# Kernel optimization log

Hardware: AMD Instinct MI355X
Metric: run time of the kernel (lower is better)

Reference implementation:

```python
import jax, jax.numpy as jnp
import numpy as np

D_MODEL = 1024
H = 16
D_K = D_MODEL // H

def setup_inputs() -> dict:
    key = jax.random.key(0)
    ks = jax.random.split(key, 7)
    B, S = 4, 2048
    q = jax.random.normal(ks[0], (B, S, D_MODEL), dtype=jnp.float32)
    k = jax.random.normal(ks[1], (B, S, D_MODEL), dtype=jnp.float32)
    v = jax.random.normal(ks[2], (B, S, D_MODEL), dtype=jnp.float32)
    scale = 1.0 / np.sqrt(D_MODEL)
    w_q = jax.random.normal(ks[3], (D_MODEL, D_MODEL), dtype=jnp.float32) * scale
    w_k = jax.random.normal(ks[4], (D_MODEL, D_MODEL), dtype=jnp.float32) * scale
    w_v = jax.random.normal(ks[5], (D_MODEL, D_MODEL), dtype=jnp.float32) * scale
    w_o = jax.random.normal(ks[6], (D_MODEL, D_MODEL), dtype=jnp.float32) * scale
    return {"q": q, "k": k, "v": v, "w_q": w_q, "w_k": w_k, "w_v": w_v, "w_o": w_o}

def reference(q, k, v, w_q, w_k, w_v, w_o):
    B, S, _ = q.shape
    # Linear layers (no bias): x @ W^T, weights stored torch-style [out, in]
    def proj(x, w):
        y = jnp.einsum('bsd,ed->bse', x, w)
        return y.reshape(B, -1, H, D_K).transpose(0, 2, 1, 3)  # [B,H,S,d_k]
    query = proj(q, w_q)
    key_ = proj(k, w_k)
    value = proj(v, w_v)
    scores = jnp.einsum('bhqd,bhkd->bhqk', query, key_) / jnp.sqrt(jnp.float32(D_K))
    attn = jax.nn.softmax(scores, axis=-1)  # dropout p=0 -> identity
    x = jnp.einsum('bhqk,bhkd->bhqd', attn, value)
    x = x.transpose(0, 2, 1, 3).reshape(B, S, H * D_K)
    return jnp.einsum('bsd,ed->bse', x, w_o)
```

## Files before the change

kernel.cpp:

```cpp
#include <hip/hip_runtime.h>

typedef unsigned short ushort_t;
typedef __attribute__((ext_vector_type(8))) short bf16x8;
typedef __attribute__((ext_vector_type(4))) float f32x4;
typedef __attribute__((ext_vector_type(16))) float f32x16;
typedef __attribute__((ext_vector_type(4))) unsigned short ushort4v;
typedef __attribute__((ext_vector_type(4))) unsigned int uint4v;

__device__ __forceinline__ ushort_t f2bf(float f) {
  unsigned u = __float_as_uint(f);
  u += 0x7FFFu + ((u >> 16) & 1u);
  return (ushort_t)(u >> 16);
}

__device__ __forceinline__ unsigned cvt_pk(float lo, float hi) {
  unsigned r;
  asm("v_cvt_pk_bf16_f32 %0, %1, %2" : "=v"(r) : "v"(lo), "v"(hi));
  return r;
}

__device__ __forceinline__ float fast_exp2(float x) {
  float r;
  asm("v_exp_f32 %0, %1" : "=v"(r) : "v"(x));
  return r;
}

__device__ __forceinline__ void gload16(ushort_t* lds, const ushort_t* g) {
  __builtin_amdgcn_global_load_lds(
      (const __attribute__((address_space(1))) unsigned int*)g,
      (__attribute__((address_space(3))) unsigned int*)lds, 16, 0, 0);
}

__global__ void cast_w4(const float* __restrict__ s0, const float* __restrict__ s1,
                        const float* __restrict__ s2, const float* __restrict__ s3,
                        ushort_t* __restrict__ dst, int n4) {
  int i = blockIdx.x * blockDim.x + threadIdx.x;
  if (i >= n4) return;
  int z = blockIdx.y;
  const float* s = (z == 0) ? s0 : (z == 1) ? s1 : (z == 2) ? s2 : s3;
  float4 f = ((const float4*)s)[i];
  ushort4v o;
  o.x = f2bf(f.x); o.y = f2bf(f.y); o.z = f2bf(f.z); o.w = f2bf(f.w);
  ((ushort4v*)(dst + (size_t)z * n4 * 4))[i] = o;
}

__global__ __launch_bounds__(256, 2)
void qkv_gemm(const float* __restrict__ qa, const float* __restrict__ ka,
              const float* __restrict__ va, const ushort_t* __restrict__ Wb,
              ushort_t* __restrict__ QKp, ushort_t* __restrict__ Vt,
              float qscale) {
  const int M = 8192, N = 1024, K = 1024;
  __shared__ __align__(16) ushort_t As[2][128 * 64];
  __shared__ __align__(16) ushort_t Bs[2][128 * 64];
  const int tid = threadIdx.x;
  const int wave = tid >> 6, lane = tid & 63;
  const int wr = wave >> 1, wc = wave & 1;
  const int frow = lane & 15, g = lane >> 4;
  const int r8 = lane >> 3, c8 = lane & 7;
  const int m0 = blockIdx.x * 128, n0 = blockIdx.y * 128;
  const int z = blockIdx.z;

  const float* Asrc = (z == 0) ? qa : (z == 1) ? ka : va;
  const float scale = (z == 0) ? qscale : 1.0f;

  f32x4 acc[4][4] = {};

  const int sc = (c8 ^ r8) << 3;
  const ushort_t* Bb = Wb + (size_t)z * N * K + (size_t)(n0 + wave * 32 + r8) * K + sc;
  const float* Af = Asrc + (size_t)(m0 + wave * 32 + r8) * K + sc;

  float aF[32];
  auto loadA = [&](int t) {
#pragma unroll
    for (int j = 0; j < 4; ++j) {
      *(float4*)&aF[j * 8]     = *(const float4*)(Af + (size_t)j * 8 * K + t * 64);
      *(float4*)&aF[j * 8 + 4] = *(const float4*)(Af + (size_t)j * 8 * K + t * 64 + 4);
    }
  };
  auto writeA = [&](int sel) {
    ushort_t* AsW = &As[sel][(wave * 32) * 64];
#pragma unroll
    for (int j = 0; j < 4; ++j) {
      uint4v w;
      w[0] = cvt_pk(aF[j * 8 + 0], aF[j * 8 + 1]);
      w[1] = cvt_pk(aF[j * 8 + 2], aF[j * 8 + 3]);
      w[2] = cvt_pk(aF[j * 8 + 4], aF[j * 8 + 5]);
      w[3] = cvt_pk(aF[j * 8 + 6], aF[j * 8 + 7]);
      *(uint4v*)&AsW[j * 8 * 64 + lane * 8] = w;
    }
  };
  auto stageB = [&](int t, int sel) {
    ushort_t* BsW = &Bs[sel][(wave * 32) * 64];
#pragma unroll
    for (int j = 0; j < 4; ++j)
      gload16(BsW + j * 8 * 64, Bb + (size_t)j * 8 * K + t * 64);
  };

  loadA(0);
  writeA(0);
  stageB(0, 0);
  loadA(1);
  __syncthreads();

  const int NT = K / 64;
  for (int t = 0; t < NT; ++t) {
    const int cur = t & 1, nxt = cur ^ 1;
    if (t < NT - 1) {
      writeA(nxt);
      stageB(t + 1, nxt);
      if (t < NT - 2) loadA(t + 2);
    }

    bf16x8 af[4][2], bfr[4][2];
#pragma unroll
    for (int mi = 0; mi < 4; ++mi) {
      int row = wr * 64 + mi * 16 + frow;
#pragma unroll
      for (int ki = 0; ki < 2; ++ki)
        af[mi][ki] = *(const bf16x8*)&As[cur][row * 64 + (((ki * 4 + g) ^ (row & 7)) << 3)];
    }
#pragma unroll
    for (int nf = 0; nf < 4; ++nf) {
      int row = wc * 64 + nf * 16 + frow;
#pragma unroll
      for (int ki = 0; ki < 2; ++ki)
        bfr[nf][ki] = *(const bf16x8*)&Bs[cur][row * 64 + (((ki * 4 + g) ^ (row & 7)) << 3)];
    }
#pragma unroll
    for (int ki = 0; ki < 2; ++ki)
#pragma unroll
      for (int mi = 0; mi < 4; ++mi)
#pragma unroll
        for (int nf = 0; nf < 4; ++nf)
          acc[mi][nf] = __builtin_amdgcn_mfma_f32_16x16x32_bf16(
              af[mi][ki], bfr[nf][ki], acc[mi][nf], 0, 0, 0);

    __syncthreads();
  }

#pragma unroll
  for (int mi = 0; mi < 4; ++mi)
#pragma unroll
    for (int nf = 0; nf < 4; ++nf)
#pragma unroll
      for (int r = 0; r < 4; ++r) {
        int m = m0 + wr * 64 + mi * 16 + g * 4 + r;
        int n = n0 + wc * 64 + nf * 16 + frow;
        float v = acc[mi][nf][r] * scale;
        if (z == 2) {
          int b = m >> 11, s = m & 2047, h = n >> 6, dk = n & 63;
          Vt[(((size_t)((b * 16 + h) * 64 + dk)) << 11) + s] = f2bf(v);
        } else {
          QKp[(size_t)z * M * N + (size_t)m * N + n] = f2bf(v);
        }
      }
}

__global__ __launch_bounds__(256, 2)
void gemm_out(const ushort_t* __restrict__ A, const ushort_t* __restrict__ B,
              float* __restrict__ Cp, int M, int N, int K) {
  __shared__ __align__(16) ushort_t As[2][128 * 64];
  __shared__ __align__(16) ushort_t Bs[2][128 * 64];
  const int tid = threadIdx.x;
  const int wave = tid >> 6, lane = tid & 63;
  const int wr = wave >> 1, wc = wave & 1;
  const int frow = lane & 15, g = lane >> 4;
  const int r8 = lane >> 3, c8 = lane & 7;
  const int m0 = blockIdx.x * 128, n0 = blockIdx.y * 128;

  f32x4 acc[4][4] = {};

  const int sc = (c8 ^ r8) << 3;
  const ushort_t* Ab = A + (size_t)(m0 + wave * 32 + r8) * K + sc;
  const ushort_t* Bb = B + (size_t)(n0 + wave * 32 + r8) * K + sc;

  auto stage = [&](int t, int sel) {
    ushort_t* AsW = &As[sel][(wave * 32) * 64];
    ushort_t* BsW = &Bs[sel][(wave * 32) * 64];
#pragma unroll
    for (int j = 0; j < 4; ++j) {
      gload16(AsW + j * 8 * 64, Ab + (size_t)j * 8 * K + t * 64);
      gload16(BsW + j * 8 * 64, Bb + (size_t)j * 8 * K + t * 64);
    }
  };

  stage(0, 0);
  __syncthreads();

  const int NT = K / 64;
  for (int t = 0; t < NT; ++t) {
    const int cur = t & 1;
    if (t < NT - 1) stage(t + 1, cur ^ 1);

    bf16x8 af[4][2], bfr[4][2];
#pragma unroll
    for (int mi = 0; mi < 4; ++mi) {
      int row = wr * 64 + mi * 16 + frow;
#pragma unroll
      for (int ki = 0; ki < 2; ++ki)
        af[mi][ki] = *(const bf16x8*)&As[cur][row * 64 + (((ki * 4 + g) ^ (row & 7)) << 3)];
    }
#pragma unroll
    for (int nf = 0; nf < 4; ++nf) {
      int row = wc * 64 + nf * 16 + frow;
#pragma unroll
      for (int ki = 0; ki < 2; ++ki)
        bfr[nf][ki] = *(const bf16x8*)&Bs[cur][row * 64 + (((ki * 4 + g) ^ (row & 7)) << 3)];
    }
#pragma unroll
    for (int ki = 0; ki < 2; ++ki)
#pragma unroll
      for (int mi = 0; mi < 4; ++mi)
#pragma unroll
        for (int nf = 0; nf < 4; ++nf)
          acc[mi][nf] = __builtin_amdgcn_mfma_f32_16x16x32_bf16(
              af[mi][ki], bfr[nf][ki], acc[mi][nf], 0, 0, 0);

    __syncthreads();
  }

#pragma unroll
  for (int mi = 0; mi < 4; ++mi)
#pragma unroll
    for (int nf = 0; nf < 4; ++nf)
#pragma unroll
      for (int r = 0; r < 4; ++r) {
        int m = m0 + wr * 64 + mi * 16 + g * 4 + r;
        int n = n0 + wc * 64 + nf * 16 + frow;
        Cp[(size_t)m * N + n] = acc[mi][nf][r];
      }
}

__global__ __launch_bounds__(256, 2)
void attn_kernel(const ushort_t* __restrict__ Qp, const ushort_t* __restrict__ Kp,
                 const ushort_t* __restrict__ Vt, ushort_t* __restrict__ Xb) {
  __shared__ __align__(16) ushort_t Ks[2][64 * 64];
  __shared__ __align__(16) ushort_t Vs[2][64 * 64];

  const int tid = threadIdx.x;
  const int wave = tid >> 6, lane = tid & 63;
  const int l31 = lane & 31, h = lane >> 5;
  const int f8 = lane >> 3, c8 = lane & 7;

  const int d = blockIdx.x;
  const int bh = ((d >> 6) << 3) | (d & 7);
  const int qt = (d >> 3) & 7;
  const int b = bh >> 4, hd = bh & 15;
  const int q0 = qt * 256 + wave * 64;

  bf16x8 qf[2][4];
  {
    const ushort_t* qb_ = Qp + (size_t)(b * 2048 + q0 + l31) * 1024 + hd * 64 + 8 * h;
#pragma unroll
    for (int qb = 0; qb < 2; ++qb)
#pragma unroll
      for (int ki = 0; ki < 4; ++ki)
        qf[qb][ki] = *(const bf16x8*)(qb_ + (size_t)(qb * 32) * 1024 + 16 * ki);
  }

  f32x16 oacc[2][2] = {};
  float ls[2][4] = {};

  const ushort_t* Kbase = Kp + (size_t)(b * 2048) * 1024 + hd * 64;
  const ushort_t* Vbase = Vt + ((size_t)(bh * 64) << 11);

  auto stage = [&](int kt, int sel) {
#pragma unroll
    for (int j = 0; j < 2; ++j) {
      int row = wave * 16 + j * 8 + f8;
      gload16(&Ks[sel][(wave * 16 + j * 8) * 64],
              Kbase + (size_t)(kt * 64 + row) * 1024 + ((c8 ^ f8) << 3));
      gload16(&Vs[sel][(wave * 16 + j * 8) * 64],
              Vbase + ((size_t)row << 11) + kt * 64 + ((c8 ^ f8) << 3));
    }
  };

  stage(0, 0);

  for (int kt = 0; kt < 32; ++kt) {
    const int cur = kt & 1;
    __syncthreads();
    if (kt < 31) stage(kt + 1, cur ^ 1);

    bf16x8 kf[2][4];
#pragma unroll
    for (int c = 0; c < 2; ++c)
#pragma unroll
      for (int ki = 0; ki < 4; ++ki) {
        int row = c * 32 + l31;
        kf[c][ki] = *(const bf16x8*)&Ks[cur][row * 64 + (((2 * ki + h) ^ (row & 7)) << 3)];
      }
    bf16x8 vf[4][2];
#pragma unroll
    for (int kc = 0; kc < 4; ++kc)
#pragma unroll
      for (int db = 0; db < 2; ++db) {
        int row = db * 32 + l31;
        vf[kc][db] = *(const bf16x8*)&Vs[cur][row * 64 + (((2 * kc + h) ^ (row & 7)) << 3)];
      }

#pragma unroll
    for (int qb = 0; qb < 2; ++qb) {
      f32x16 sacc[2];
      __builtin_amdgcn_s_setprio(1);
#pragma unroll
      for (int c = 0; c < 2; ++c) {
        sacc[c] = __builtin_amdgcn_mfma_f32_32x32x16_bf16(
            kf[c][0], qf[qb][0], (f32x16)(0.0f), 0, 0, 0);
#pragma unroll
        for (int ki = 1; ki < 4; ++ki)
          sacc[c] = __builtin_amdgcn_mfma_f32_32x32x16_bf16(
              kf[c][ki], qf[qb][ki], sacc[c], 0, 0, 0);
      }
      __builtin_amdgcn_s_setprio(0);

#pragma unroll
      for (int c = 0; c < 2; ++c)
#pragma unroll
        for (int r = 0; r < 16; r += 4) {
          float p0 = fast_exp2(sacc[c][r]);
          float p1 = fast_exp2(sacc[c][r + 1]);
          float p2 = fast_exp2(sacc[c][r + 2]);
          float p3 = fast_exp2(sacc[c][r + 3]);
          sacc[c][r] = p0; sacc[c][r + 1] = p1;
          sacc[c][r + 2] = p2; sacc[c][r + 3] = p3;
          ls[qb][0] += p0; ls[qb][1] += p1; ls[qb][2] += p2; ls[qb][3] += p3;
        }

      bf16x8 pfrag[4];
#pragma unroll
      for (int kc = 0; kc < 4; ++kc) {
        const int e = 2 * kc, o = 2 * kc + 1;
        const int ce = e >> 2, me = e & 3, co = o >> 2, mo = o & 3;
        unsigned x0, x1, y0, y1;
        x0 = cvt_pk(sacc[ce][4 * me],     sacc[ce][4 * me + 1]);
        x1 = cvt_pk(sacc[ce][4 * me + 2], sacc[ce][4 * me + 3]);
        y0 = cvt_pk(sacc[co][4 * mo],     sacc[co][4 * mo + 1]);
        y1 = cvt_pk(sacc[co][4 * mo + 2], sacc[co][4 * mo + 3]);
        asm("v_permlane32_swap_b32 %0, %1" : "+v"(x0), "+v"(y0));
        asm("v_permlane32_swap_b32 %0, %1" : "+v"(x1), "+v"(y1));
        uint4v pu; pu[0] = x0; pu[1] = x1; pu[2] = y0; pu[3] = y1;
        pfrag[kc] = __builtin_bit_cast(bf16x8, pu);
      }

      __builtin_amdgcn_s_setprio(1);
#pragma unroll
      for (int kc = 0; kc < 4; ++kc)
#pragma unroll
        for (int db = 0; db < 2; ++db)
          oacc[qb][db] = __builtin_amdgcn_mfma_f32_32x32x16_bf16(
              pfrag[kc], vf[kc][db], oacc[qb][db], 0, 0, 0);
      __builtin_amdgcn_s_setprio(0);
    }
  }

#pragma unroll
  for (int qb = 0; qb < 2; ++qb) {
    float lsum = (ls[qb][0] + ls[qb][1]) + (ls[qb][2] + ls[qb][3]);
    float lf = lsum + __shfl_xor(lsum, 32, 64);
    float linv = 1.0f / lf;
#pragma unroll
    for (int db = 0; db < 2; ++db)
#pragma unroll
      for (int r = 0; r < 16; ++r) {
        int qrow = (r & 3) + 8 * (r >> 2) + 4 * h;
        float li = __shfl(linv, qrow, 64);
        int grow = b * 2048 + q0 + qb * 32 + qrow;
        int gcol = hd * 64 + db * 32 + l31;
        Xb[(size_t)grow * 1024 + gcol] = f2bf(oacc[qb][db][r] * li);
      }
  }
}

extern "C" void kernel_launch(void* const* d_in, const int* in_sizes, int n_in,
                              void* d_out, int out_size, void* d_ws, size_t ws_size,
                              hipStream_t stream) {
  const float* q = (const float*)d_in[0];
  const float* k = (const float*)d_in[1];
  const float* v = (const float*)d_in[2];
  const float* wq = (const float*)d_in[3];
  const float* wk = (const float*)d_in[4];
  const float* wv = (const float*)d_in[5];
  const float* wo = (const float*)d_in[6];

  const int M = 8192, D = 1024;
  const size_t MD = (size_t)M * D;
  const size_t DD = (size_t)D * D;

  ushort_t* ws = (ushort_t*)d_ws;
  ushort_t* buf0 = ws;
  ushort_t* Qp = buf0 + MD;
  ushort_t* Kp = Qp + MD;
  ushort_t* Vt = Kp + MD;
  ushort_t* wqb = Vt + MD;
  ushort_t* wob = wqb + 3 * DD;

  {
    int n4 = (int)(DD / 4);
    dim3 gw((n4 + 255) / 256, 4);
    cast_w4<<<gw, 256, 0, stream>>>(wq, wk, wv, wo, wqb, n4);
  }

  {
    dim3 gq(M / 128, D / 128, 3);
    qkv_gemm<<<gq, 256, 0, stream>>>(q, k, v, wqb, Qp, Vt,
                                     0.125f * 1.44269504f);
  }

  attn_kernel<<<512, 256, 0, stream>>>(Qp, Kp, Vt, buf0);

  dim3 gg(M / 128, D / 128);
  gemm_out<<<gg, 256, 0, stream>>>(buf0, wob, (float*)d_out, M, D, D);
}
```

Measured before the change: 192.9 us.

## Halve attention q-tile per block and compute row sums via MFMA with ones

Each wave now handles 32 query rows instead of 64, so each block covers 128 queries and the grid doubles to 1024 blocks. This raises parallelism and lowers register pressure, but K/V tiles are reused across half as many queries, which doubles staging traffic per unit of work. The softmax denominator is no longer built from scalar adds of exponentials. It is accumulated by an extra MFMA of the probabilities against a ones vector, giving per-row sums directly in the output layout and removing the final shuffles. That sum now comes from bf16-rounded probabilities, which matches the numerator's precision.

```diff
diff --git a/kernel.cpp b/kernel.cpp
--- a/kernel.cpp
+++ b/kernel.cpp
@@ -243,23 +243,25 @@
   const int f8 = lane >> 3, c8 = lane & 7;
 
   const int d = blockIdx.x;
-  const int bh = ((d >> 6) << 3) | (d & 7);
-  const int qt = (d >> 3) & 7;
+  const int bh = ((d >> 7) << 3) | (d & 7);
+  const int qt = (d >> 3) & 15;
   const int b = bh >> 4, hd = bh & 15;
-  const int q0 = qt * 256 + wave * 64;
-
-  bf16x8 qf[2][4];
+  const int q0 = qt * 128 + wave * 32;
+
+  bf16x8 qf[4];
   {
     const ushort_t* qb_ = Qp + (size_t)(b * 2048 + q0 + l31) * 1024 + hd * 64 + 8 * h;
 #pragma unroll
-    for (int qb = 0; qb < 2; ++qb)
-#pragma unroll
-      for (int ki = 0; ki < 4; ++ki)
-        qf[qb][ki] = *(const bf16x8*)(qb_ + (size_t)(qb * 32) * 1024 + 16 * ki);
-  }
-
-  f32x16 oacc[2][2] = {};
-  float ls[2][4] = {};
+    for (int ki = 0; ki < 4; ++ki)
+      qf[ki] = *(const bf16x8*)(qb_ + 16 * ki);
+  }
+
+  const short one_bf = (short)0x3F80;
+  const bf16x8 vones = {one_bf, one_bf, one_bf, one_bf,
+                        one_bf, one_bf, one_bf, one_bf};
+
+  f32x16 oacc[2] = {};
+  f32x16 lones = {};
 
   const ushort_t* Kbase = Kp + (size_t)(b * 2048) * 1024 + hd * 64;
   const ushort_t* Vbase = Vt + ((size_t)(bh * 64) << 11);
@@ -299,77 +301,70 @@
         vf[kc][db] = *(const bf16x8*)&Vs[cur][row * 64 + (((2 * kc + h) ^ (row & 7)) << 3)];
       }
 
-#pragma unroll
-    for (int qb = 0; qb < 2; ++qb) {
-      f32x16 sacc[2];
-      __builtin_amdgcn_s_setprio(1);
-#pragma unroll
-      for (int c = 0; c < 2; ++c) {
+    f32x16 sacc[2];
+    __builtin_amdgcn_s_setprio(1);
+#pragma unroll
+    for (int c = 0; c < 2; ++c) {
+      sacc[c] = __builtin_amdgcn_mfma_f32_32x32x16_bf16(
+          kf[c][0], qf[0], (f32x16)(0.0f), 0, 0, 0);
+#pragma unroll
+      for (int ki = 1; ki < 4; ++ki)
         sacc[c] = __builtin_amdgcn_mfma_f32_32x32x16_bf16(
-            kf[c][0], qf[qb][0], (f32x16)(0.0f), 0, 0, 0);
-#pragma unroll
-        for (int ki = 1; ki < 4; ++ki)
-          sacc[c] = __builtin_amdgcn_mfma_f32_32x32x16_bf16(
-              kf[c][ki], qf[qb][ki], sacc[c], 0, 0, 0);
+            kf[c][ki], qf[ki], sacc[c], 0, 0, 0);
+    }
+    __builtin_amdgcn_s_setprio(0);
+
+#pragma unroll
+    for (int c = 0; c < 2; ++c)
+#pragma unroll
+      for (int r = 0; r < 16; r += 4) {
+        sacc[c][r]     = fast_exp2(sacc[c][r]);
+        sacc[c][r + 1] = fast_exp2(sacc[c][r + 1]);
+        sacc[c][r + 2] = fast_exp2(sacc[c][r + 2]);
+        sacc[c][r + 3] = fast_exp2(sacc[c][r + 3]);
       }
-      __builtin_amdgcn_s_setprio(0);
-
-#pragma unroll
-      for (int c = 0; c < 2; ++c)
-#pragma unroll
-        for (int r = 0; r < 16; r += 4) {
-          float p0 = fast_exp2(sacc[c][r]);
-          float p1 = fast_exp2(sacc[c][r + 1]);
-          float p2 = fast_exp2(sacc[c][r + 2]);
-          float p3 = fast_exp2(sacc[c][r + 3]);
-          sacc[c][r] = p0; sacc[c][r + 1] = p1;
-          sacc[c][r + 2] = p2; sacc[c][r + 3] = p3;
-          ls[qb][0] += p0; ls[qb][1] += p1; ls[qb][2] += p2; ls[qb][3] += p3;
-        }
-
-      bf16x8 pfrag[4];
-#pragma unroll
-      for (int kc = 0; kc < 4; ++kc) {
-        const int e = 2 * kc, o = 2 * kc + 1;
-        const int ce = e >> 2, me = e & 3, co = o >> 2, mo = o & 3;
-        unsigned x0, x1, y0, y1;
-        x0 = cvt_pk(sacc[ce][4 * me],     sacc[ce][4 * me + 1]);
-        x1 = cvt_pk(sacc[ce][4 * me + 2], sacc[ce][4 * me + 3]);
-        y0 = cvt_pk(sacc[co][4 * mo],     sacc[co][4 * mo + 1]);
-        y1 = cvt_pk(sacc[co][4 * mo + 2], sacc[co][4 * mo + 3]);
-        asm("v_permlane32_swap_b32 %0, %1" : "+v"(x0), "+v"(y0));
-        asm("v_permlane32_swap_b32 %0, %1" : "+v"(x1), "+v"(y1));
-        uint4v pu; pu[0] = x0; pu[1] = x1; pu[2] = y0; pu[3] = y1;
-        pfrag[kc] = __builtin_bit_cast(bf16x8, pu);
-      }
-
-      __builtin_amdgcn_s_setprio(1);
-#pragma unroll
-      for (int kc = 0; kc < 4; ++kc)
-#pragma unroll
-        for (int db = 0; db < 2; ++db)
-          oacc[qb][db] = __builtin_amdgcn_mfma_f32_32x32x16_bf16(
-              pfrag[kc], vf[kc][db], oacc[qb][db], 0, 0, 0);
-      __builtin_amdgcn_s_setprio(0);
-    }
-  }
-
-#pragma unroll
-  for (int qb = 0; qb < 2; ++qb) {
-    float lsum = (ls[qb][0] + ls[qb][1]) + (ls[qb][2] + ls[qb][3]);
-    float lf = lsum + __shfl_xor(lsum, 32, 64);
-    float linv = 1.0f / lf;
-#pragma unroll
-    for (int db = 0; db < 2; ++db)
-#pragma unroll
-      for (int r = 0; r < 16; ++r) {
-        int qrow = (r & 3) + 8 * (r >> 2) + 4 * h;
-        float li = __shfl(linv, qrow, 64);
-        int grow = b * 2048 + q0 + qb * 32 + qrow;
-        int gcol = hd * 64 + db * 32 + l31;
-        Xb[(size_t)grow * 1024 + gcol] = f2bf(oacc[qb][db][r] * li);
-      }
-  }
+
+    bf16x8 pfrag[4];
+#pragma unroll
+    for (int kc = 0; kc < 4; ++kc) {
+      const int e = 2 * kc, o = 2 * kc + 1;
+      const int ce = e >> 2, me = e & 3, co = o >> 2, mo = o & 3;
+      unsigned x0, x1, y0, y1;
+      x0 = cvt_pk(sacc[ce][4 * me],     sacc[ce][4 * me + 1]);
+      x1 = cvt_pk(sacc[ce][4 * me + 2], sacc[ce][4 * me + 3]);
+      y0 = cvt_pk(sacc[co][4 * mo],     sacc[co][4 * mo + 1]);
+      y1 = cvt_pk(sacc[co][4 * mo + 2], sacc[co][4 * mo + 3]);
+      asm("v_permlane32_swap_b32 %0, %1" : "+v"(x0), "+v"(y0));
+      asm("v_permlane32_swap_b32 %0, %1" : "+v"(x1), "+v"(y1));
+      uint4v pu; pu[0] = x0; pu[1] = x1; pu[2] = y0; pu[3] = y1;
+      pfrag[kc] = __builtin_bit_cast(bf16x8, pu);
+    }
+
+    __builtin_amdgcn_s_setprio(1);
+#pragma unroll
+    for (int kc = 0; kc < 4; ++kc) {
+      oacc[0] = __builtin_amdgcn_mfma_f32_32x32x16_bf16(
+          pfrag[kc], vf[kc][0], oacc[0], 0, 0, 0);
+      oacc[1] = __builtin_amdgcn_mfma_f32_32x32x16_bf16(
+          pfrag[kc], vf[kc][1], oacc[1], 0, 0, 0);
+      lones = __builtin_amdgcn_mfma_f32_32x32x16_bf16(
+          pfrag[kc], vones, lones, 0, 0, 0);
+    }
+    __builtin_amdgcn_s_setprio(0);
+  }
+
+  float linv[16];
+#pragma unroll
+  for (int r = 0; r < 16; ++r) linv[r] = 1.0f / lones[r];
+#pragma unroll
+  for (int db = 0; db < 2; ++db)
+#pragma unroll
+    for (int r = 0; r < 16; ++r) {
+      int qrow = (r & 3) + 8 * (r >> 2) + 4 * h;
+      int grow = b * 2048 + q0 + qrow;
+      int gcol = hd * 64 + db * 32 + l31;
+      Xb[(size_t)grow * 1024 + gcol] = f2bf(oacc[db][r] * linv[r]);
+    }
 }
 
 extern "C" void kernel_launch(void* const* d_in, const int* in_sizes, int n_in,
@@ -407,7 +402,7 @@
                                      0.125f * 1.44269504f);
   }
 
-  attn_kernel<<<512, 256, 0, stream>>>(Qp, Kp, Vt, buf0);
+  attn_kernel<<<1024, 256, 0, stream>>>(Qp, Kp, Vt, buf0);
 
   dim3 gg(M / 128, D / 128);
   gemm_out<<<gg, 256, 0, stream>>>(buf0, wob, (float*)d_out, M, D, D);
```

After: 212.1 us. 1.1x slower.

## Deepen K/V LDS ring to four stages and compute row sums via MFMA

Applied to the files above, without the earlier changes.

The attention kernel's K/V shared-memory buffers grow from a double buffer to a four-slot ring. Two tiles are staged per barrier, which halves the number of __syncthreads calls and gives loads more time in flight. The softmax row sums are no longer accumulated with VALU adds on fp32 values; an extra MFMA against a vector of bf16 ones produces them in the output layout, which also removes the final cross-lane shuffles. This doubles LDS use per block, which may reduce occupancy, adds one MFMA per two in the PV step, and sums the bf16-rounded probabilities rather than the fp32 ones.

```diff
diff --git a/kernel.cpp b/kernel.cpp
--- a/kernel.cpp
+++ b/kernel.cpp
@@ -234,8 +234,8 @@
 __global__ __launch_bounds__(256, 2)
 void attn_kernel(const ushort_t* __restrict__ Qp, const ushort_t* __restrict__ Kp,
                  const ushort_t* __restrict__ Vt, ushort_t* __restrict__ Xb) {
-  __shared__ __align__(16) ushort_t Ks[2][64 * 64];
-  __shared__ __align__(16) ushort_t Vs[2][64 * 64];
+  __shared__ __align__(16) ushort_t Ks[4][64 * 64];
+  __shared__ __align__(16) ushort_t Vs[4][64 * 64];
 
   const int tid = threadIdx.x;
   const int wave = tid >> 6, lane = tid & 63;
@@ -258,8 +258,12 @@
         qf[qb][ki] = *(const bf16x8*)(qb_ + (size_t)(qb * 32) * 1024 + 16 * ki);
   }
 
+  const short one_bf = (short)0x3F80;
+  const bf16x8 vones = {one_bf, one_bf, one_bf, one_bf,
+                        one_bf, one_bf, one_bf, one_bf};
+
   f32x16 oacc[2][2] = {};
-  float ls[2][4] = {};
+  f32x16 lones[2] = {};
 
   const ushort_t* Kbase = Kp + (size_t)(b * 2048) * 1024 + hd * 64;
   const ushort_t* Vbase = Vt + ((size_t)(bh * 64) << 11);
@@ -276,11 +280,17 @@
   };
 
   stage(0, 0);
+  stage(1, 1);
 
   for (int kt = 0; kt < 32; ++kt) {
-    const int cur = kt & 1;
-    __syncthreads();
-    if (kt < 31) stage(kt + 1, cur ^ 1);
+    if ((kt & 1) == 0) {
+      __syncthreads();
+      if (kt < 30) {
+        stage(kt + 2, (kt + 2) & 3);
+        stage(kt + 3, (kt + 3) & 3);
+      }
+    }
+    const int cur = kt & 3;
 
     bf16x8 kf[2][4];
 #pragma unroll
@@ -318,13 +328,10 @@
       for (int c = 0; c < 2; ++c)
 #pragma unroll
         for (int r = 0; r < 16; r += 4) {
-          float p0 = fast_exp2(sacc[c][r]);
-          float p1 = fast_exp2(sacc[c][r + 1]);
-          float p2 = fast_exp2(sacc[c][r + 2]);
-          float p3 = fast_exp2(sacc[c][r + 3]);
-          sacc[c][r] = p0; sacc[c][r + 1] = p1;
-          sacc[c][r + 2] = p2; sacc[c][r + 3] = p3;
-          ls[qb][0] += p0; ls[qb][1] += p1; ls[qb][2] += p2; ls[qb][3] += p3;
+          sacc[c][r]     = fast_exp2(sacc[c][r]);
+          sacc[c][r + 1] = fast_exp2(sacc[c][r + 1]);
+          sacc[c][r + 2] = fast_exp2(sacc[c][r + 2]);
+          sacc[c][r + 3] = fast_exp2(sacc[c][r + 3]);
         }
 
       bf16x8 pfrag[4];
@@ -345,29 +352,31 @@
 
       __builtin_amdgcn_s_setprio(1);
 #pragma unroll
-      for (int kc = 0; kc < 4; ++kc)
-#pragma unroll
-        for (int db = 0; db < 2; ++db)
-          oacc[qb][db] = __builtin_amdgcn_mfma_f32_32x32x16_bf16(
-              pfrag[kc], vf[kc][db], oacc[qb][db], 0, 0, 0);
+      for (int kc = 0; kc < 4; ++kc) {
+        oacc[qb][0] = __builtin_amdgcn_mfma_f32_32x32x16_bf16(
+            pfrag[kc], vf[kc][0], oacc[qb][0], 0, 0, 0);
+        oacc[qb][1] = __builtin_amdgcn_mfma_f32_32x32x16_bf16(
+            pfrag[kc], vf[kc][1], oacc[qb][1], 0, 0, 0);
+        lones[qb] = __builtin_amdgcn_mfma_f32_32x32x16_bf16(
+            pfrag[kc], vones, lones[qb], 0, 0, 0);
+      }
       __builtin_amdgcn_s_setprio(0);
     }
   }
 
 #pragma unroll
   for (int qb = 0; qb < 2; ++qb) {
-    float lsum = (ls[qb][0] + ls[qb][1]) + (ls[qb][2] + ls[qb][3]);
-    float lf = lsum + __shfl_xor(lsum, 32, 64);
-    float linv = 1.0f / lf;
+    float linv[16];
+#pragma unroll
+    for (int r = 0; r < 16; ++r) linv[r] = 1.0f / lones[qb][r];
 #pragma unroll
     for (int db = 0; db < 2; ++db)
 #pragma unroll
       for (int r = 0; r < 16; ++r) {
         int qrow = (r & 3) + 8 * (r >> 2) + 4 * h;
-        float li = __shfl(linv, qrow, 64);
         int grow = b * 2048 + q0 + qb * 32 + qrow;
         int gcol = hd * 64 + db * 32 + l31;
-        Xb[(size_t)grow * 1024 + gcol] = f2bf(oacc[qb][db][r] * li);
+        Xb[(size_t)grow * 1024 + gcol] = f2bf(oacc[qb][db][r] * linv[r]);
       }
   }
 }
```

Result: slower. 198.0 us (+2.7%).
